# Kernel optimization log

Hardware: AMD Instinct MI355X
Metric: run time of the kernel (lower is better)

## Reference

```python
import jax, jax.numpy as jnp
import numpy as np
import math

D_MODEL = 1024
N_HEADS = 16
D_FF = 4096
EPS = 1e-6
NEG = -1e9


def layer_norm(x, gamma, beta):
    # Faithful to torch: std with Bessel correction (ddof=1), eps added to std.
    mean = jnp.mean(x, axis=-1, keepdims=True)
    std = jnp.std(x, axis=-1, keepdims=True, ddof=1)
    return gamma * ((x - mean) / (std + EPS)) + beta


def mha(x_q, x_kv, wq, bq, wk, bk, wv, bv, wo, bo, mask):
    B, Sq, D = x_q.shape
    Sk = x_kv.shape[1]
    dk = D // N_HEADS
    q = (x_q @ wq + bq).reshape(B, Sq, N_HEADS, dk).transpose(0, 2, 1, 3)
    k = (x_kv @ wk + bk).reshape(B, Sk, N_HEADS, dk).transpose(0, 2, 1, 3)
    v = (x_kv @ wv + bv).reshape(B, Sk, N_HEADS, dk).transpose(0, 2, 1, 3)
    scores = jnp.einsum('bhqd,bhkd->bhqk', q, k) / math.sqrt(dk)
    scores = jnp.where(mask == 0, NEG, scores)
    attn = jax.nn.softmax(scores, axis=-1)
    out = jnp.einsum('bhqk,bhkd->bhqd', attn, v)
    out = out.transpose(0, 2, 1, 3).reshape(B, Sq, D)
    return out @ wo + bo


def setup_inputs() -> dict:
    key = jax.random.key(0)
    ks = jax.random.split(key, 24)
    B, S, D = 2, 2048, D_MODEL
    sc = 0.02
    lin = lambda k, i, o: jax.random.normal(k, (i, o), jnp.float32) * sc
    inp = {
        'x': jax.random.normal(ks[0], (B, S, D), jnp.float32),
        'encoder_output': jax.random.normal(ks[1], (B, S, D), jnp.float32),
        'src_mask': jnp.ones((1, 1, 1, S), jnp.int32),
        'tgt_mask': jnp.tril(jnp.ones((S, S), jnp.int32))[None, None],
        # self-attention params
        'sa_wq': lin(ks[2], D, D), 'sa_bq': jnp.zeros((D,), jnp.float32),
        'sa_wk': lin(ks[3], D, D), 'sa_bk': jnp.zeros((D,), jnp.float32),
        'sa_wv': lin(ks[4], D, D), 'sa_bv': jnp.zeros((D,), jnp.float32),
        'sa_wo': lin(ks[5], D, D), 'sa_bo': jnp.zeros((D,), jnp.float32),
        # cross-attention params
        'ca_wq': lin(ks[6], D, D), 'ca_bq': jnp.zeros((D,), jnp.float32),
        'ca_wk': lin(ks[7], D, D), 'ca_bk': jnp.zeros((D,), jnp.float32),
        'ca_wv': lin(ks[8], D, D), 'ca_bv': jnp.zeros((D,), jnp.float32),
        'ca_wo': lin(ks[9], D, D), 'ca_bo': jnp.zeros((D,), jnp.float32),
        # feed-forward params
        'ff_w1': lin(ks[10], D, D_FF), 'ff_b1': jnp.zeros((D_FF,), jnp.float32),
        'ff_w2': lin(ks[11], D_FF, D), 'ff_b2': jnp.zeros((D,), jnp.float32),
        # layer norms (3 residual connections)
        'n1_g': jnp.ones((D,), jnp.float32), 'n1_b': jnp.zeros((D,), jnp.float32),
        'n2_g': jnp.ones((D,), jnp.float32), 'n2_b': jnp.zeros((D,), jnp.float32),
        'n3_g': jnp.ones((D,), jnp.float32), 'n3_b': jnp.zeros((D,), jnp.float32),
    }
    return inp


def reference(x, encoder_output, src_mask, tgt_mask,
              sa_wq, sa_bq, sa_wk, sa_bk, sa_wv, sa_bv, sa_wo, sa_bo,
              ca_wq, ca_bq, ca_wk, ca_bk, ca_wv, ca_bv, ca_wo, ca_bo,
              ff_w1, ff_b1, ff_w2, ff_b2,
              n1_g, n1_b, n2_g, n2_b, n3_g, n3_b):
    # Pre-norm residual block 1: self-attention (dropout=0 -> identity)
    h = layer_norm(x, n1_g, n1_b)
    x = x + mha(h, h, sa_wq, sa_bq, sa_wk, sa_bk, sa_wv, sa_bv, sa_wo, sa_bo, tgt_mask)
    # Block 2: cross-attention over encoder output
    h = layer_norm(x, n2_g, n2_b)
    x = x + mha(h, encoder_output, ca_wq, ca_bq, ca_wk, ca_bk, ca_wv, ca_bv, ca_wo, ca_bo, src_mask)
    # Block 3: feed-forward
    h = layer_norm(x, n3_g, n3_b)
    ff = jax.nn.relu(h @ ff_w1 + ff_b1) @ ff_w2 + ff_b2
    return x + ff
```

## Files before the change

### kernel.cpp

```cpp
#include <hip/hip_runtime.h>

typedef short short8 __attribute__((ext_vector_type(8)));
typedef float f32x4 __attribute__((ext_vector_type(4)));

#define SEQ 2048
#define QSCALE 0.18033688011112042f
#define PSHIFT 20.0f
#define EXP2(x) __builtin_amdgcn_exp2f(x)

#define GLDS(g, l) __builtin_amdgcn_global_load_lds( \
    (const __attribute__((address_space(1))) unsigned int*)(g), \
    (__attribute__((address_space(3))) unsigned int*)(l), 16, 0, 0)

__device__ __forceinline__ unsigned short f2bf(float f) {
    unsigned int u = __builtin_bit_cast(unsigned int, f);
    unsigned int r = (u + 0x7fffu + ((u >> 16) & 1u)) >> 16;
    return (unsigned short)r;
}

__global__ __launch_bounds__(256)
void wtrans8_kernel(const float* w0, const float* w1, const float* w2, const float* w3,
                    const float* w4, const float* w5, const float* w6, const float* w7,
                    unsigned short* __restrict__ outbase)
{
    const float* Ws[8] = {w0, w1, w2, w3, w4, w5, w6, w7};
    const float* __restrict__ W = Ws[blockIdx.z];
    unsigned short* __restrict__ Wt = outbase + (size_t)blockIdx.z * 1024 * 1024;
    __shared__ float t[32][33];
    const int tx = threadIdx.x & 31;
    const int ty = threadIdx.x >> 5;
    const int nb = blockIdx.x * 32;
    const int kb = blockIdx.y * 32;
#pragma unroll
    for (int i = 0; i < 4; i++)
        t[ty + i * 8][tx] = W[(size_t)(kb + ty + i * 8) * 1024 + nb + tx];
    __syncthreads();
#pragma unroll
    for (int i = 0; i < 4; i++)
        Wt[(size_t)(nb + ty + i * 8) * 1024 + kb + tx] = f2bf(t[tx][ty + i * 8]);
}

__global__ __launch_bounds__(256)
void wtrans_kernel(const float* __restrict__ W, unsigned short* __restrict__ Wt,
                   int Kd, int Nd)
{
    __shared__ float t[32][33];
    const int tx = threadIdx.x & 31;
    const int ty = threadIdx.x >> 5;
    const int nb = blockIdx.x * 32;
    const int kb = blockIdx.y * 32;
#pragma unroll
    for (int i = 0; i < 4; i++)
        t[ty + i * 8][tx] = W[(size_t)(kb + ty + i * 8) * Nd + nb + tx];
    __syncthreads();
#pragma unroll
    for (int i = 0; i < 4; i++)
        Wt[(size_t)(nb + ty + i * 8) * Kd + kb + tx] = f2bf(t[tx][ty + i * 8]);
}

__global__ __launch_bounds__(256)
void cvt_kernel(const float* __restrict__ in, unsigned short* __restrict__ out, int n)
{
    int i = (blockIdx.x * 256 + threadIdx.x) * 4;
    if (i < n) {
        float4 v = *(const float4*)(in + i);
        ushort4 o;
        o.x = f2bf(v.x); o.y = f2bf(v.y); o.z = f2bf(v.z); o.w = f2bf(v.w);
        *(ushort4*)(out + i) = o;
    }
}

__global__ __launch_bounds__(256)
void ln_kernel(const float* __restrict__ x, const float* __restrict__ g,
               const float* __restrict__ bb, unsigned short* __restrict__ out)
{
    const int D = 1024;
    const int row = blockIdx.x;
    const float* xr = x + (size_t)row * D;
    float v[4];
    float s = 0.f, ss = 0.f;
#pragma unroll
    for (int i = 0; i < 4; i++) {
        v[i] = xr[threadIdx.x + i * 256];
        s += v[i];
        ss += v[i] * v[i];
    }
#pragma unroll
    for (int off = 1; off < 64; off <<= 1) {
        s  += __shfl_xor(s,  off, 64);
        ss += __shfl_xor(ss, off, 64);
    }
    __shared__ float red[8];
    const int wave = threadIdx.x >> 6;
    if ((threadIdx.x & 63) == 0) { red[wave] = s; red[4 + wave] = ss; }
    __syncthreads();
    s  = red[0] + red[1] + red[2] + red[3];
    ss = red[4] + red[5] + red[6] + red[7];
    float mean = s / D;
    float var  = fmaxf((ss - s * mean) / (D - 1), 0.f);
    float inv  = 1.f / (sqrtf(var) + 1e-6f);
#pragma unroll
    for (int i = 0; i < 4; i++) {
        int c = threadIdx.x + i * 256;
        out[(size_t)row * D + c] = f2bf(g[c] * (v[i] - mean) * inv + bb[c]);
    }
}

template <int MODE>
__global__ __launch_bounds__(256)
void gemm_kernel(const unsigned short* __restrict__ A,
                 const unsigned short* __restrict__ A2,
                 const unsigned short* __restrict__ Wt,
                 const float* __restrict__ b0,
                 const float* __restrict__ b1,
                 const float* __restrict__ b2,
                 unsigned short* __restrict__ o0,
                 unsigned short* __restrict__ o1,
                 unsigned short* __restrict__ o2,
                 int M, int N, int K)
{
    __shared__ unsigned short As[128 * 32];
    __shared__ unsigned short Bs[128 * 32];
    const int tid  = threadIdx.x;
    const int lane = tid & 63;
    const int wv   = tid >> 6;
    const int quad = lane >> 4;
    const int l16  = lane & 15;
    const int m0 = blockIdx.y * 128;
    const int n0 = blockIdx.x * 128;
    const int wm = (wv >> 1) << 6;
    const int wn = (wv & 1) << 6;
    const int sect = (MODE == 1) ? (n0 >> 10) : 0;
    const unsigned short* Asel = (MODE == 1 && sect != 0) ? A2 : A;

    const int srow0 = wv * 32 + (lane >> 2);
    const int srow1 = srow0 + 16;
    const int scol8 = (lane & 3) * 8;
    unsigned short* asw0 = &As[(wv * 2 + 0) * 512];
    unsigned short* asw1 = &As[(wv * 2 + 1) * 512];
    unsigned short* bsw0 = &Bs[(wv * 2 + 0) * 512];
    unsigned short* bsw1 = &Bs[(wv * 2 + 1) * 512];
    const unsigned short* Ag0 = Asel + (size_t)(m0 + srow0) * K + scol8;
    const unsigned short* Ag1 = Asel + (size_t)(m0 + srow1) * K + scol8;
    const unsigned short* Bg0 = Wt   + (size_t)(n0 + srow0) * K + scol8;
    const unsigned short* Bg1 = Wt   + (size_t)(n0 + srow1) * K + scol8;

    f32x4 acc[4][4];
#pragma unroll
    for (int i = 0; i < 4; i++)
#pragma unroll
        for (int j = 0; j < 4; j++) acc[i][j] = f32x4{0.f, 0.f, 0.f, 0.f};

    for (int k0 = 0; k0 < K; k0 += 32) {
        GLDS(Ag0 + k0, asw0);
        GLDS(Ag1 + k0, asw1);
        GLDS(Bg0 + k0, bsw0);
        GLDS(Bg1 + k0, bsw1);
        __syncthreads();
        short8 af[4], bfr[4];
#pragma unroll
        for (int i = 0; i < 4; i++)
            af[i] = *(const short8*)(&As[(wm + i * 16 + l16) * 32 + quad * 8]);
#pragma unroll
        for (int i = 0; i < 4; i++)
            bfr[i] = *(const short8*)(&Bs[(wn + i * 16 + l16) * 32 + quad * 8]);
#pragma unroll
        for (int mi = 0; mi < 4; mi++)
#pragma unroll
            for (int ni = 0; ni < 4; ni++)
                acc[mi][ni] = __builtin_amdgcn_mfma_f32_16x16x32_bf16(
                    af[mi], bfr[ni], acc[mi][ni], 0, 0, 0);
        __syncthreads();
    }

    if (MODE == 1) {
        const float* bias = (sect == 0) ? b0 : ((sect == 1) ? b1 : b2);
        if (sect == 2) {
#pragma unroll
            for (int mi = 0; mi < 4; mi++)
#pragma unroll
                for (int ni = 0; ni < 4; ni++) {
                    const int cc = (n0 + wn + ni * 16 + l16) & 1023;
                    const int h = cc >> 6, d = cc & 63;
                    const float bv = bias[cc];
                    const int rowg = m0 + wm + mi * 16 + quad * 4;
                    const int b = rowg >> 11, s = rowg & 2047;
                    ushort4 o4;
                    o4.x = f2bf(acc[mi][ni][0] + bv);
                    o4.y = f2bf(acc[mi][ni][1] + bv);
                    o4.z = f2bf(acc[mi][ni][2] + bv);
                    o4.w = f2bf(acc[mi][ni][3] + bv);
                    *(ushort4*)&o2[((size_t)(b * 16 + h) * 64 + d) * SEQ + s] = o4;
                }
        } else {
            unsigned short* dst = (sect == 0) ? o0 : o1;
            const float scl = (sect == 0) ? QSCALE : 1.0f;
#pragma unroll
            for (int mi = 0; mi < 4; mi++)
#pragma unroll
                for (int ni = 0; ni < 4; ni++) {
                    const int cc = (n0 + wn + ni * 16 + l16) & 1023;
                    const int h = cc >> 6, d = cc & 63;
                    const float bv = bias[cc];
#pragma unroll
                    for (int r = 0; r < 4; r++) {
                        const int rowg = m0 + wm + mi * 16 + quad * 4 + r;
                        const int b = rowg >> 11, s = rowg & 2047;
                        float v = (acc[mi][ni][r] + bv) * scl;
                        dst[((size_t)(b * 16 + h) * SEQ + s) * 64 + d] = f2bf(v);
                    }
                }
        }
    } else {
#pragma unroll
        for (int mi = 0; mi < 4; mi++)
#pragma unroll
            for (int ni = 0; ni < 4; ni++) {
                const int colg = n0 + wn + ni * 16 + l16;
                const float bv = b0[colg];
#pragma unroll
                for (int r = 0; r < 4; r++) {
                    const int rowg = m0 + wm + mi * 16 + quad * 4 + r;
                    float v = acc[mi][ni][r] + bv;
                    o0[(size_t)rowg * N + colg] = f2bf(fmaxf(v, 0.f));
                }
            }
    }
}

__global__ __launch_bounds__(256)
void gemm64_kernel(const unsigned short* __restrict__ A,
                   const unsigned short* __restrict__ Wt,
                   const float* __restrict__ b0,
                   const float* __restrict__ res,
                   float* __restrict__ outf,
                   int M, int N, int K)
{
    __shared__ unsigned short As[64 * 32];
    __shared__ unsigned short Bs[128 * 32];
    const int tid  = threadIdx.x;
    const int lane = tid & 63;
    const int wv   = tid >> 6;
    const int quad = lane >> 4;
    const int l16  = lane & 15;
    const int m0 = blockIdx.y * 64;
    const int n0 = blockIdx.x * 128;
    const int wm = (wv >> 1) << 5;
    const int wn = (wv & 1) << 6;

    const int arow  = wv * 16 + (lane >> 2);
    const int brow0 = wv * 32 + (lane >> 2);
    const int brow1 = brow0 + 16;
    const int scol8 = (lane & 3) * 8;
    unsigned short* asw  = &As[wv * 512];
    unsigned short* bsw0 = &Bs[(wv * 2 + 0) * 512];
    unsigned short* bsw1 = &Bs[(wv * 2 + 1) * 512];
    const unsigned short* Ag  = A  + (size_t)(m0 + arow)  * K + scol8;
    const unsigned short* Bg0 = Wt + (size_t)(n0 + brow0) * K + scol8;
    const unsigned short* Bg1 = Wt + (size_t)(n0 + brow1) * K + scol8;

    f32x4 acc[2][4];
#pragma unroll
    for (int i = 0; i < 2; i++)
#pragma unroll
        for (int j = 0; j < 4; j++) acc[i][j] = f32x4{0.f, 0.f, 0.f, 0.f};

    for (int k0 = 0; k0 < K; k0 += 32) {
        GLDS(Ag + k0, asw);
        GLDS(Bg0 + k0, bsw0);
        GLDS(Bg1 + k0, bsw1);
        __syncthreads();
        short8 af[2], bfr[4];
#pragma unroll
        for (int i = 0; i < 2; i++)
            af[i] = *(const short8*)(&As[(wm + i * 16 + l16) * 32 + quad * 8]);
#pragma unroll
        for (int i = 0; i < 4; i++)
            bfr[i] = *(const short8*)(&Bs[(wn + i * 16 + l16) * 32 + quad * 8]);
#pragma unroll
        for (int mi = 0; mi < 2; mi++)
#pragma unroll
            for (int ni = 0; ni < 4; ni++)
                acc[mi][ni] = __builtin_amdgcn_mfma_f32_16x16x32_bf16(
                    af[mi], bfr[ni], acc[mi][ni], 0, 0, 0);
        __syncthreads();
    }

#pragma unroll
    for (int mi = 0; mi < 2; mi++)
#pragma unroll
        for (int ni = 0; ni < 4; ni++) {
            const int colg = n0 + wn + ni * 16 + l16;
            const float bv = b0[colg];
#pragma unroll
            for (int r = 0; r < 4; r++) {
                const int rowg = m0 + wm + mi * 16 + quad * 4 + r;
                float v = acc[mi][ni][r] + bv;
                outf[(size_t)rowg * N + colg] = v + res[(size_t)rowg * N + colg];
            }
        }
}

template <bool CAUSAL>
__global__ __launch_bounds__(256, 2)
void attn4_kernel(const unsigned short* __restrict__ Q,
                  const unsigned short* __restrict__ K,
                  const unsigned short* __restrict__ VT,
                  unsigned short* __restrict__ O)
{
    __shared__ unsigned short Ks[128 * 72];
    __shared__ unsigned short Vt[64 * 136];
    __shared__ unsigned short Ps[4][32 * 136];
    __shared__ float sumS[4][32];
    const int tid  = threadIdx.x;
    const int lane = tid & 63;
    const int wave = tid >> 6;
    const int quad = lane >> 4;
    const int l16  = lane & 15;
    const int bh = blockIdx.y;
    const int qb = (CAUSAL && (bh & 16)) ? (15 - (int)blockIdx.x) : (int)blockIdx.x;
    const int q0 = qb * 128;
    const size_t baseK = (size_t)bh * SEQ * 64;
    const size_t baseV = (size_t)bh * 64 * SEQ;

    short8 aq[2][2];
#pragma unroll
    for (int qs = 0; qs < 2; qs++) {
        const unsigned short* qp =
            Q + baseK + (size_t)(q0 + wave * 32 + qs * 16 + l16) * 64 + quad * 8;
        aq[qs][0] = *(const short8*)(qp);
        aq[qs][1] = *(const short8*)(qp + 32);
    }
    f32x4 acc[4][2];
#pragma unroll
    for (int i = 0; i < 4; i++)
#pragma unroll
        for (int j = 0; j < 2; j++) acc[i][j] = f32x4{0.f, 0.f, 0.f, 0.f};
    float lsum[2][4] = {{0.f, 0.f, 0.f, 0.f}, {0.f, 0.f, 0.f, 0.f}};

    const int nkb = CAUSAL ? (qb + 1) : (SEQ / 128);
    const int krow = tid >> 1;
    const int kc   = (tid & 1) * 32;
    const int vrow = tid >> 2;
    const int vc   = (tid & 3) * 32;
    const unsigned short* kg = K  + baseK + (size_t)krow * 64 + kc;
    const unsigned short* vg = VT + baseV + (size_t)vrow * SEQ + vc;

    short8 kr0 = *(const short8*)(kg),      kr1 = *(const short8*)(kg + 8);
    short8 kr2 = *(const short8*)(kg + 16), kr3 = *(const short8*)(kg + 24);
    short8 vr0 = *(const short8*)(vg),      vr1 = *(const short8*)(vg + 8);
    short8 vr2 = *(const short8*)(vg + 16), vr3 = *(const short8*)(vg + 24);

    for (int kb = 0; kb < nkb; kb++) {
        __syncthreads();
        *(short8*)&Ks[krow * 72 + kc]      = kr0;
        *(short8*)&Ks[krow * 72 + kc + 8]  = kr1;
        *(short8*)&Ks[krow * 72 + kc + 16] = kr2;
        *(short8*)&Ks[krow * 72 + kc + 24] = kr3;
        *(short8*)&Vt[vrow * 136 + vc]      = vr0;
        *(short8*)&Vt[vrow * 136 + vc + 8]  = vr1;
        *(short8*)&Vt[vrow * 136 + vc + 16] = vr2;
        *(short8*)&Vt[vrow * 136 + vc + 24] = vr3;
        if (kb + 1 < nkb) {
            const unsigned short* kg2 = kg + (size_t)(kb + 1) * 128 * 64;
            const unsigned short* vg2 = vg + (size_t)(kb + 1) * 128;
            kr0 = *(const short8*)(kg2);      kr1 = *(const short8*)(kg2 + 8);
            kr2 = *(const short8*)(kg2 + 16); kr3 = *(const short8*)(kg2 + 24);
            vr0 = *(const short8*)(vg2);      vr1 = *(const short8*)(vg2 + 8);
            vr2 = *(const short8*)(vg2 + 16); vr3 = *(const short8*)(vg2 + 24);
        }
        __syncthreads();

        const bool maskTile = CAUSAL && (kb == nkb - 1);
#pragma unroll
        for (int qs = 0; qs < 2; qs++) {
            f32x4 scf[8];
#pragma unroll
            for (int nt = 0; nt < 8; nt++) {
                f32x4 z = f32x4{0.f, 0.f, 0.f, 0.f};
#pragma unroll
                for (int c = 0; c < 2; c++) {
                    short8 bk = *(const short8*)(&Ks[(nt * 16 + l16) * 72 + c * 32 + quad * 8]);
                    z = __builtin_amdgcn_mfma_f32_16x16x32_bf16(aq[qs][c], bk, z, 0, 0, 0);
                }
                scf[nt] = z;
            }
            if (maskTile) {
                const int qg = q0 + wave * 32 + qs * 16 + quad * 4;
                const int k0 = kb * 128;
#pragma unroll
                for (int nt = 0; nt < 8; nt++) {
                    const int kg_ = k0 + nt * 16 + l16;
#pragma unroll
                    for (int r = 0; r < 4; r++)
                        if (kg_ > qg + r) scf[nt][r] = -1e9f;
                }
            }
#pragma unroll
            for (int nt = 0; nt < 8; nt++)
#pragma unroll
                for (int r = 0; r < 4; r++) {
                    float pv = EXP2(scf[nt][r] - PSHIFT);
                    lsum[qs][r] += pv;
                    Ps[wave][(qs * 16 + quad * 4 + r) * 136 +
                             ((nt * 16 + l16) ^ (quad * 8))] = f2bf(pv);
                }
        }
        const int pswz = 8 * (quad ^ ((l16 >> 2) & 3));
#pragma unroll
        for (int c = 0; c < 4; c++) {
            short8 av[4];
#pragma unroll
            for (int mi = 0; mi < 4; mi++)
                av[mi] = *(const short8*)(&Vt[(mi * 16 + l16) * 136 + c * 32 + quad * 8]);
#pragma unroll
            for (int qs = 0; qs < 2; qs++) {
                short8 bp = *(const short8*)(&Ps[wave][(qs * 16 + l16) * 136 + c * 32 + pswz]);
#pragma unroll
                for (int mi = 0; mi < 4; mi++)
                    acc[mi][qs] = __builtin_amdgcn_mfma_f32_16x16x32_bf16(av[mi], bp, acc[mi][qs], 0, 0, 0);
            }
        }
    }
#pragma unroll
    for (int qs = 0; qs < 2; qs++)
#pragma unroll
        for (int r = 0; r < 4; r++) {
#pragma unroll
            for (int off = 1; off < 16; off <<= 1)
                lsum[qs][r] += __shfl_xor(lsum[qs][r], off, 64);
        }
    if (l16 == 0) {
#pragma unroll
        for (int qs = 0; qs < 2; qs++)
#pragma unroll
            for (int r = 0; r < 4; r++)
                sumS[wave][qs * 16 + quad * 4 + r] = lsum[qs][r];
    }
    __syncthreads();
    const int b = bh >> 4, h = bh & 15;
#pragma unroll
    for (int qs = 0; qs < 2; qs++) {
        const float rcpL = 1.f / sumS[wave][qs * 16 + l16];
        const int qg = q0 + wave * 32 + qs * 16 + l16;
#pragma unroll
        for (int mi = 0; mi < 4; mi++) {
            ushort4 o4;
            o4.x = f2bf(acc[mi][qs][0] * rcpL);
            o4.y = f2bf(acc[mi][qs][1] * rcpL);
            o4.z = f2bf(acc[mi][qs][2] * rcpL);
            o4.w = f2bf(acc[mi][qs][3] * rcpL);
            *(ushort4*)&O[(size_t)(b * SEQ + qg) * 1024 + h * 64 + mi * 16 + quad * 4] = o4;
        }
    }
}

extern "C" void kernel_launch(void* const* d_in, const int* in_sizes, int n_in,
                              void* d_out, int out_size, void* d_ws, size_t ws_size,
                              hipStream_t stream)
{
    (void)in_sizes; (void)n_in; (void)out_size; (void)ws_size;
    const int B = 2, S = SEQ, D = 1024, DFF = 4096;
    const int M = B * S;

    const float* x     = (const float*)d_in[0];
    const float* enc   = (const float*)d_in[1];
    const float* sa_wq = (const float*)d_in[4],  *sa_bq = (const float*)d_in[5];
    const float* sa_wk = (const float*)d_in[6],  *sa_bk = (const float*)d_in[7];
    const float* sa_wv = (const float*)d_in[8],  *sa_bv = (const float*)d_in[9];
    const float* sa_wo = (const float*)d_in[10], *sa_bo = (const float*)d_in[11];
    const float* ca_wq = (const float*)d_in[12], *ca_bq = (const float*)d_in[13];
    const float* ca_wk = (const float*)d_in[14], *ca_bk = (const float*)d_in[15];
    const float* ca_wv = (const float*)d_in[16], *ca_bv = (const float*)d_in[17];
    const float* ca_wo = (const float*)d_in[18], *ca_bo = (const float*)d_in[19];
    const float* ff_w1 = (const float*)d_in[20], *ff_b1 = (const float*)d_in[21];
    const float* ff_w2 = (const float*)d_in[22], *ff_b2 = (const float*)d_in[23];
    const float* n1_g  = (const float*)d_in[24], *n1_b = (const float*)d_in[25];
    const float* n2_g  = (const float*)d_in[26], *n2_b = (const float*)d_in[27];
    const float* n3_g  = (const float*)d_in[28], *n3_b = (const float*)d_in[29];
    float* out = (float*)d_out;

    char* p = (char*)d_ws;
    auto carve = [&](size_t bytes) -> char* {
        char* r = p;
        p += (bytes + 255) & ~(size_t)255;
        return r;
    };
    unsigned short* wt8     = (unsigned short*)carve((size_t)8 * D * D * 2);
    unsigned short* wt_sqkv = wt8;
    unsigned short* wt_sao  = wt8 + (size_t)3 * D * D;
    unsigned short* wt_cqkv = wt8 + (size_t)4 * D * D;
    unsigned short* wt_cao  = wt8 + (size_t)7 * D * D;
    unsigned short* wt_ff1  = (unsigned short*)carve((size_t)D * DFF * 2);
    unsigned short* wt_ff2  = (unsigned short*)carve((size_t)DFF * D * 2);
    unsigned short* encb    = (unsigned short*)carve((size_t)M * D * 2);
    unsigned short* hb      = (unsigned short*)carve((size_t)M * D * 2);
    unsigned short* qbuf    = (unsigned short*)carve((size_t)M * D * 2);
    unsigned short* kbuf    = (unsigned short*)carve((size_t)M * D * 2);
    unsigned short* vtbuf   = (unsigned short*)carve((size_t)M * D * 2);
    unsigned short* ffh     = (unsigned short*)carve((size_t)M * DFF * 2);
    float* x1 = (float*)carve((size_t)M * D * 4);
    unsigned short* abuf = hb;
    float* x2 = out;

    dim3 blk(256);
    wtrans8_kernel<<<dim3(32, 32, 8), blk, 0, stream>>>(
        sa_wq, sa_wk, sa_wv, sa_wo, ca_wq, ca_wk, ca_wv, ca_wo, wt8);
    wtrans_kernel<<<dim3(DFF / 32, D / 32), blk, 0, stream>>>(ff_w1, wt_ff1, D, DFF);
    wtrans_kernel<<<dim3(D / 32, DFF / 32), blk, 0, stream>>>(ff_w2, wt_ff2, DFF, D);
    cvt_kernel<<<dim3(M * D / 1024), blk, 0, stream>>>(enc, encb, M * D);

    ln_kernel<<<dim3(M), blk, 0, stream>>>(x, n1_g, n1_b, hb);
    gemm_kernel<1><<<dim3(3 * D / 128, M / 128), blk, 0, stream>>>(
        hb, hb, wt_sqkv, sa_bq, sa_bk, sa_bv, qbuf, kbuf, vtbuf, M, 3 * D, D);
    attn4_kernel<true><<<dim3(S / 128, B * 16), blk, 0, stream>>>(qbuf, kbuf, vtbuf, abuf);
    gemm64_kernel<<<dim3(D / 128, M / 64), blk, 0, stream>>>(
        abuf, wt_sao, sa_bo, x, x1, M, D, D);

    ln_kernel<<<dim3(M), blk, 0, stream>>>(x1, n2_g, n2_b, hb);
    gemm_kernel<1><<<dim3(3 * D / 128, M / 128), blk, 0, stream>>>(
        hb, encb, wt_cqkv, ca_bq, ca_bk, ca_bv, qbuf, kbuf, vtbuf, M, 3 * D, D);
    attn4_kernel<false><<<dim3(S / 128, B * 16), blk, 0, stream>>>(qbuf, kbuf, vtbuf, abuf);
    gemm64_kernel<<<dim3(D / 128, M / 64), blk, 0, stream>>>(
        abuf, wt_cao, ca_bo, x1, x2, M, D, D);

    ln_kernel<<<dim3(M), blk, 0, stream>>>(x2, n3_g, n3_b, hb);
    gemm_kernel<2><<<dim3(DFF / 128, M / 128), blk, 0, stream>>>(
        hb, hb, wt_ff1, ff_b1, nullptr, nullptr, ffh, nullptr, nullptr, M, DFF, D);
    gemm64_kernel<<<dim3(D / 128, M / 64), blk, 0, stream>>>(
        ffh, wt_ff2, ff_b2, x2, out, M, D, DFF);
}
```

Baseline: 597.1 us.

## Replace 64-row GEMM with double-buffered 128x128 tile kernel using swizzled LDS

The output-projection and FF2 GEMMs move from a 64x128 tile with BK=32 and two barriers per step to a 128x128 tile with BK=64. Global-to-LDS loads are double-buffered so the next tile's load overlaps the current MFMAs. LDS columns are XOR-swizzled to avoid bank conflicts. Each wave now holds a 4x4 MFMA accumulator grid, raising compute per load. The cost is half as many blocks, about one per CU, and lower occupancy, so latency hiding depends on the prefetch.

```diff
diff --git a/kernel.cpp b/kernel.cpp
--- a/kernel.cpp
+++ b/kernel.cpp
@@ -228,66 +228,82 @@
     }
 }
 
-__global__ __launch_bounds__(256)
-void gemm64_kernel(const unsigned short* __restrict__ A,
-                   const unsigned short* __restrict__ Wt,
-                   const float* __restrict__ b0,
-                   const float* __restrict__ res,
-                   float* __restrict__ outf,
-                   int M, int N, int K)
-{
-    __shared__ unsigned short As[64 * 32];
-    __shared__ unsigned short Bs[128 * 32];
+__global__ __launch_bounds__(256, 1)
+void gemm_db_kernel(const unsigned short* __restrict__ A,
+                    const unsigned short* __restrict__ Wt,
+                    const float* __restrict__ b0,
+                    const float* __restrict__ res,
+                    float* __restrict__ outf,
+                    int M, int N, int K)
+{
+    __shared__ unsigned short As[2][128 * 64];
+    __shared__ unsigned short Bs[2][128 * 64];
     const int tid  = threadIdx.x;
     const int lane = tid & 63;
     const int wv   = tid >> 6;
     const int quad = lane >> 4;
     const int l16  = lane & 15;
-    const int m0 = blockIdx.y * 64;
+    const int m0 = blockIdx.y * 128;
     const int n0 = blockIdx.x * 128;
-    const int wm = (wv >> 1) << 5;
+    const int wm = (wv >> 1) << 6;
     const int wn = (wv & 1) << 6;
 
-    const int arow  = wv * 16 + (lane >> 2);
-    const int brow0 = wv * 32 + (lane >> 2);
-    const int brow1 = brow0 + 16;
-    const int scol8 = (lane & 3) * 8;
-    unsigned short* asw  = &As[wv * 512];
-    unsigned short* bsw0 = &Bs[(wv * 2 + 0) * 512];
-    unsigned short* bsw1 = &Bs[(wv * 2 + 1) * 512];
-    const unsigned short* Ag  = A  + (size_t)(m0 + arow)  * K + scol8;
-    const unsigned short* Bg0 = Wt + (size_t)(n0 + brow0) * K + scol8;
-    const unsigned short* Bg1 = Wt + (size_t)(n0 + brow1) * K + scol8;
-
-    f32x4 acc[2][4];
-#pragma unroll
-    for (int i = 0; i < 2; i++)
+    const int rsub = lane >> 3;
+    const int cu8  = ((lane & 7) ^ rsub) * 8;
+    const unsigned short* Ag = A  + (size_t)(m0 + wv * 32 + rsub) * K + cu8;
+    const unsigned short* Bg = Wt + (size_t)(n0 + wv * 32 + rsub) * K + cu8;
+
+    f32x4 acc[4][4];
+#pragma unroll
+    for (int i = 0; i < 4; i++)
 #pragma unroll
         for (int j = 0; j < 4; j++) acc[i][j] = f32x4{0.f, 0.f, 0.f, 0.f};
 
-    for (int k0 = 0; k0 < K; k0 += 32) {
-        GLDS(Ag + k0, asw);
-        GLDS(Bg0 + k0, bsw0);
-        GLDS(Bg1 + k0, bsw1);
-        __syncthreads();
-        short8 af[2], bfr[4];
-#pragma unroll
-        for (int i = 0; i < 2; i++)
-            af[i] = *(const short8*)(&As[(wm + i * 16 + l16) * 32 + quad * 8]);
-#pragma unroll
-        for (int i = 0; i < 4; i++)
-            bfr[i] = *(const short8*)(&Bs[(wn + i * 16 + l16) * 32 + quad * 8]);
-#pragma unroll
-        for (int mi = 0; mi < 2; mi++)
+    const int NT = K >> 6;
+
+#pragma unroll
+    for (int r = 0; r < 4; r++) {
+        GLDS(Ag + (size_t)(r * 8) * K, &As[0][(wv * 4 + r) * 512]);
+        GLDS(Bg + (size_t)(r * 8) * K, &Bs[0][(wv * 4 + r) * 512]);
+    }
+    asm volatile("s_waitcnt vmcnt(0)" ::: "memory");
+    __builtin_amdgcn_s_barrier();
+
+    for (int i = 0; i < NT; i++) {
+        const int cur = i & 1;
+        if (i + 1 < NT) {
+            const int nb = cur ^ 1;
+            const int kb = (i + 1) << 6;
+#pragma unroll
+            for (int r = 0; r < 4; r++) {
+                GLDS(Ag + (size_t)(r * 8) * K + kb, &As[nb][(wv * 4 + r) * 512]);
+                GLDS(Bg + (size_t)(r * 8) * K + kb, &Bs[nb][(wv * 4 + r) * 512]);
+            }
+        }
+#pragma unroll
+        for (int ks = 0; ks < 2; ks++) {
+            short8 af[4], bfr[4];
+#pragma unroll
+            for (int mi = 0; mi < 4; mi++)
+                af[mi] = *(const short8*)(&As[cur][(wm + mi * 16 + l16) * 64 +
+                             (((ks * 4 + quad) ^ (l16 & 7)) * 8)]);
 #pragma unroll
             for (int ni = 0; ni < 4; ni++)
-                acc[mi][ni] = __builtin_amdgcn_mfma_f32_16x16x32_bf16(
-                    af[mi], bfr[ni], acc[mi][ni], 0, 0, 0);
-        __syncthreads();
-    }
-
-#pragma unroll
-    for (int mi = 0; mi < 2; mi++)
+                bfr[ni] = *(const short8*)(&Bs[cur][(wn + ni * 16 + l16) * 64 +
+                             (((ks * 4 + quad) ^ (l16 & 7)) * 8)]);
+#pragma unroll
+            for (int mi = 0; mi < 4; mi++)
+#pragma unroll
+                for (int ni = 0; ni < 4; ni++)
+                    acc[mi][ni] = __builtin_amdgcn_mfma_f32_16x16x32_bf16(
+                        af[mi], bfr[ni], acc[mi][ni], 0, 0, 0);
+        }
+        asm volatile("s_waitcnt vmcnt(0) lgkmcnt(0)" ::: "memory");
+        __builtin_amdgcn_s_barrier();
+    }
+
+#pragma unroll
+    for (int mi = 0; mi < 4; mi++)
 #pragma unroll
         for (int ni = 0; ni < 4; ni++) {
             const int colg = n0 + wn + ni * 16 + l16;
@@ -295,8 +311,8 @@
 #pragma unroll
             for (int r = 0; r < 4; r++) {
                 const int rowg = m0 + wm + mi * 16 + quad * 4 + r;
-                float v = acc[mi][ni][r] + bv;
-                outf[(size_t)rowg * N + colg] = v + res[(size_t)rowg * N + colg];
+                outf[(size_t)rowg * N + colg] =
+                    acc[mi][ni][r] + bv + res[(size_t)rowg * N + colg];
             }
         }
 }
@@ -514,19 +530,19 @@
     gemm_kernel<1><<<dim3(3 * D / 128, M / 128), blk, 0, stream>>>(
         hb, hb, wt_sqkv, sa_bq, sa_bk, sa_bv, qbuf, kbuf, vtbuf, M, 3 * D, D);
     attn4_kernel<true><<<dim3(S / 128, B * 16), blk, 0, stream>>>(qbuf, kbuf, vtbuf, abuf);
-    gemm64_kernel<<<dim3(D / 128, M / 64), blk, 0, stream>>>(
+    gemm_db_kernel<<<dim3(D / 128, M / 128), blk, 0, stream>>>(
         abuf, wt_sao, sa_bo, x, x1, M, D, D);
 
     ln_kernel<<<dim3(M), blk, 0, stream>>>(x1, n2_g, n2_b, hb);
     gemm_kernel<1><<<dim3(3 * D / 128, M / 128), blk, 0, stream>>>(
         hb, encb, wt_cqkv, ca_bq, ca_bk, ca_bv, qbuf, kbuf, vtbuf, M, 3 * D, D);
     attn4_kernel<false><<<dim3(S / 128, B * 16), blk, 0, stream>>>(qbuf, kbuf, vtbuf, abuf);
-    gemm64_kernel<<<dim3(D / 128, M / 64), blk, 0, stream>>>(
+    gemm_db_kernel<<<dim3(D / 128, M / 128), blk, 0, stream>>>(
         abuf, wt_cao, ca_bo, x1, x2, M, D, D);
 
     ln_kernel<<<dim3(M), blk, 0, stream>>>(x2, n3_g, n3_b, hb);
     gemm_kernel<2><<<dim3(DFF / 128, M / 128), blk, 0, stream>>>(
         hb, hb, wt_ff1, ff_b1, nullptr, nullptr, ffh, nullptr, nullptr, M, DFF, D);
-    gemm64_kernel<<<dim3(D / 128, M / 64), blk, 0, stream>>>(
+    gemm_db_kernel<<<dim3(D / 128, M / 128), blk, 0, stream>>>(
         ffh, wt_ff2, ff_b2, x2, out, M, D, DFF);
 }
```

Result: no change. 600.4 us (+0.6%).
